# Kernel optimization log

Measured on AMD Instinct MI355X. Metric: run time of the kernel, lower is better.

The kernel has to match this reference:

```python
import jax, jax.numpy as jnp
import numpy as np

B, S, T = 4, 512, 512
V, D, F, H, DK, N = 32000, 512, 2048, 8, 64, 6
PAD = 0

# sinusoidal positional encoding table, matching the torch source exactly
_pos = np.arange(max(S, T))[:, None]
_i = np.arange(D // 2)[None, :]
_ang = _pos / (10000.0 ** (2 * _i / D))
_pe = np.empty((max(S, T), D), dtype=np.float32)
_pe[:, 0::2] = np.sin(_ang)
_pe[:, 1::2] = np.cos(_ang)
PE = jnp.asarray(_pe)


def setup_inputs() -> dict:
    key = jax.random.key(0)
    ks = iter(jax.random.split(key, 64))
    s = 0.02
    w = lambda shape: jax.random.normal(next(ks), shape, jnp.float32) * s
    inp = {
        'src': jax.random.randint(next(ks), (B, S), 0, V, jnp.int32),
        'trg': jax.random.randint(next(ks), (B, T), 0, V, jnp.int32),
        'emb_src': w((V, D)).at[PAD].set(0.0),
        'emb_trg': w((V, D)).at[PAD].set(0.0),
        # encoder stacks (leading axis = layer)
        'enc_wq': w((N, D, H * DK)), 'enc_wk': w((N, D, H * DK)),
        'enc_wv': w((N, D, H * DK)), 'enc_wo': w((N, H * DK, D)),
        'enc_ln1_g': jnp.ones((N, D)), 'enc_ln1_b': jnp.zeros((N, D)),
        'enc_w1': w((N, D, F)), 'enc_b1': jnp.zeros((N, F)),
        'enc_w2': w((N, F, D)), 'enc_b2': jnp.zeros((N, D)),
        'enc_ln2_g': jnp.ones((N, D)), 'enc_ln2_b': jnp.zeros((N, D)),
        # decoder stacks
        'dec_wq': w((N, D, H * DK)), 'dec_wk': w((N, D, H * DK)),
        'dec_wv': w((N, D, H * DK)), 'dec_wo': w((N, H * DK, D)),
        'dec_ln1_g': jnp.ones((N, D)), 'dec_ln1_b': jnp.zeros((N, D)),
        'dec_cq': w((N, D, H * DK)), 'dec_ck': w((N, D, H * DK)),
        'dec_cv': w((N, D, H * DK)), 'dec_co': w((N, H * DK, D)),
        'dec_ln2_g': jnp.ones((N, D)), 'dec_ln2_b': jnp.zeros((N, D)),
        'dec_w1': w((N, D, F)), 'dec_b1': jnp.zeros((N, F)),
        'dec_w2': w((N, F, D)), 'dec_b2': jnp.zeros((N, D)),
        'dec_ln3_g': jnp.ones((N, D)), 'dec_ln3_b': jnp.zeros((N, D)),
        'proj': w((D, V)),
    }
    return inp


def _ln(x, g, b, eps=1e-5):
    m = x.mean(-1, keepdims=True)
    v = ((x - m) ** 2).mean(-1, keepdims=True)
    return (x - m) * jax.lax.rsqrt(v + eps) * g + b


def _mha(xq, xkv, wq, wk, wv, wo, mask):
    b, lq, _ = xq.shape
    lk = xkv.shape[1]
    q = (xq @ wq).reshape(b, lq, H, DK).transpose(0, 2, 1, 3)   # bhqd
    k = (xkv @ wk).reshape(b, lk, H, DK).transpose(0, 2, 1, 3)  # bhkd
    v = (xkv @ wv).reshape(b, lk, H, DK).transpose(0, 2, 1, 3)  # bhkd
    scores = jnp.einsum('bhqd,bhkd->bhqk', q, k)
    scores = jnp.where(mask, -jnp.inf, scores)
    attn = jax.nn.softmax(scores * (DK ** -0.5), axis=-1)
    out = jnp.einsum('bhqk,bhkd->bhqd', attn, v)
    out = out.transpose(0, 2, 1, 3).reshape(b, lq, H * DK)
    return out @ wo


def _ffn(x, w1, b1, w2, b2):
    return jax.nn.relu(x @ w1 + b1) @ w2 + b2


def reference(src, trg, emb_src, emb_trg,
              enc_wq, enc_wk, enc_wv, enc_wo, enc_ln1_g, enc_ln1_b,
              enc_w1, enc_b1, enc_w2, enc_b2, enc_ln2_g, enc_ln2_b,
              dec_wq, dec_wk, dec_wv, dec_wo, dec_ln1_g, dec_ln1_b,
              dec_cq, dec_ck, dec_cv, dec_co, dec_ln2_g, dec_ln2_b,
              dec_w1, dec_b1, dec_w2, dec_b2, dec_ln3_g, dec_ln3_b,
              proj):
    scale = D ** 0.5
    src_pad = (src == PAD)[:, None, None, :]                 # [B,1,1,S]
    trg_pad = (trg == PAD)[:, None, None, :]                 # [B,1,1,T]
    causal = jnp.triu(jnp.ones((T, T), bool), 1)[None, None]  # [1,1,T,T]
    trg_mask = trg_pad | causal

    # encoder (dropout = identity in eval)
    x = emb_src[src] * scale + PE[None, :S]

    def enc_step(h, p):
        wq, wk, wv, wo, g1, b1, w1, bb1, w2, bb2, g2, b2 = p
        h = _ln(h + _mha(h, h, wq, wk, wv, wo, src_pad), g1, b1)
        h = _ln(h + _ffn(h, w1, bb1, w2, bb2), g2, b2)
        return h, None

    x_enc, _ = jax.lax.scan(enc_step, x,
        (enc_wq, enc_wk, enc_wv, enc_wo, enc_ln1_g, enc_ln1_b,
         enc_w1, enc_b1, enc_w2, enc_b2, enc_ln2_g, enc_ln2_b))

    # decoder
    y = emb_trg[trg] * scale + PE[None, :T]

    def dec_step(h, p):
        (wq, wk, wv, wo, g1, b1, cq, ck, cv, co, g2, b2,
         w1, bb1, w2, bb2, g3, b3) = p
        h = _ln(h + _mha(h, h, wq, wk, wv, wo, trg_mask), g1, b1)
        h = _ln(h + _mha(h, x_enc, cq, ck, cv, co, src_pad), g2, b2)
        h = _ln(h + _ffn(h, w1, bb1, w2, bb2), g3, b3)
        return h, None

    y, _ = jax.lax.scan(dec_step, y,
        (dec_wq, dec_wk, dec_wv, dec_wo, dec_ln1_g, dec_ln1_b,
         dec_cq, dec_ck, dec_cv, dec_co, dec_ln2_g, dec_ln2_b,
         dec_w1, dec_b1, dec_w2, dec_b2, dec_ln3_g, dec_ln3_b))

    return y @ proj  # [B, T, trg_vocab]
```

## Files before the change

### kernel.cpp

```cpp
#include <hip/hip_runtime.h>
#include <math.h>

#define BBATCH 4
#define SS 512
#define DDIM 512
#define FFN 2048
#define NHEAD 8
#define DHEAD 64
#define NL 6
#define NVOC 32000
#define MTOK (BBATCH*SS)
#define PAD_ID 0
#define MSZE ((size_t)MTOK * DDIM)

typedef unsigned short u16;
typedef __attribute__((ext_vector_type(8))) short short8;
typedef __attribute__((ext_vector_type(4))) float f32x4;

__device__ __forceinline__ u16 f2bf(float f) {
    union { float f; unsigned u; } v; v.f = f;
    unsigned r = ((v.u >> 16) & 1u) + 0x7fffu;
    return (u16)((v.u + r) >> 16);
}

// ... 67 lines not shown
    auto comp = [&](int t) {
        const u16* as = AsB + (t & 3) * (BM * 32);
        const u16* bs = BsB + (t & 3) * (BN * 32);
        short8 af[MF], bf[NF];
        #pragma unroll
        for (int m = 0; m < MF; m++) {
            int row = wr * (BM / 2) + m * 16 + (lane & 15);
            int slot = ((lane >> 4) << 4) ^ ((row & 3) << 4);
            af[m] = *(const short8*)&as[row * 32 + (slot >> 1)];
        }
        #pragma unroll
        for (int n = 0; n < NF; n++) {
            int row = wc * (BN / 2) + n * 16 + (lane & 15);
            int slot = ((lane >> 4) << 4) ^ ((row & 3) << 4);
            bf[n] = *(const short8*)&bs[row * 32 + (slot >> 1)];
        }
        __builtin_amdgcn_s_setprio(1);
        #pragma unroll
        for (int m = 0; m < MF; m++)
            #pragma unroll
            for (int n = 0; n < NF; n++)
                acc[m][n] = __builtin_amdgcn_mfma_f32_16x16x32_bf16(af[m], bf[n], acc[m][n], 0, 0, 0);
        __builtin_amdgcn_s_setprio(0);
    };

    const int nt = K / 32;
    issue(0); issue(1); issue(2);
    int t = 0;
    for (; t < nt - 2; ++t) {
        waitv<2 * LPT>();
        rawbar();
        if (t + 3 < nt) issue(t + 3);
        comp(t);
    }
    waitv<LPT>(); rawbar(); comp(nt - 2);
    waitv<0>();   rawbar(); comp(nt - 1);

    const int crow = row0 + wr * (BM / 2);
    const int ccol = col0 + wc * (BN / 2);
    #pragma unroll
    for (int m = 0; m < MF; m++) {
        #pragma unroll
        for (int n = 0; n < NF; n++) {
            int col = ccol + n * 16 + (lane & 15);
            float bv = BIAS ? bias[col] : 0.0f;
            #pragma unroll
            for (int i = 0; i < 4; i++) {
                int row = crow + m * 16 + ((lane >> 4) << 2) + i;
                float v = acc[m][n][i] + bv;
                if (RELU) v = fmaxf(v, 0.0f);
                if (OUTBF) ((u16*)Cv)[(size_t)row * ldc + col] = f2bf(v);
                else       ((float*)Cv)[(size_t)row * ldc + col] = v;
            }
        }
    }
}

template<int BM, int BN, int OUTBF, int RELU, int BIAS, int SWZ = 0>
__global__ __launch_bounds__(256) void mgemm(
    const u16* __restrict__ A, int lda, size_t aSb, size_t aSh,
    const u16* __restrict__ B, int ldb, size_t bSb, size_t bSh,
    void* __restrict__ Cv, int ldc, size_t cSb, size_t cSh,
    int K, const float* __restrict__ bias)
{
    __shared__ __align__(16) u16 As[4 * BM * 32];
    __shared__ __align__(16) u16 Bs[4 * BN * 32];
    int bx = blockIdx.x, by = blockIdx.y;
    if (SWZ) {
        int nwg = gridDim.x * gridDim.y;
        int lin = by * gridDim.x + bx;
        int cpx = nwg >> 3;
        int s = (lin & 7) * cpx + (lin >> 3);
        bx = s % gridDim.x; by = s / gridDim.x;
    }
    const int zb = blockIdx.z >> 3, zh = blockIdx.z & 7;
    const u16* Ab = A + (size_t)zb * aSb + (size_t)zh * aSh;
    const u16* Bb = B + (size_t)zb * bSb + (size_t)zh * bSh;
    void* Cb = OUTBF ? (void*)((u16*)Cv + (size_t)zb * cSb + (size_t)zh * cSh)
                     : (void*)((float*)Cv + (size_t)zb * cSb + (size_t)zh * cSh);
    gemm_core<BM, BN, OUTBF, RELU, BIAS>(As, Bs, Ab, lda, Bb, ldb, Cb, ldc,
                                          by * BM, bx * BN, K, bias);
}

template<int BM, int BN>
__global__ __launch_bounds__(256) void mgemm_dual(
    const u16* __restrict__ A1, int lda1, const u16* __restrict__ B1, int ldb1,
    u16* __restrict__ C1, int ldc1, int nx1, int nblk1,
    const u16* __restrict__ A2, int lda2, const u16* __restrict__ B2, int ldb2,
    u16* __restrict__ C2, int ldc2, int nx2,
    int K)
{
    __shared__ __align__(16) u16 As[4 * BM * 32];
    __shared__ __align__(16) u16 Bs[4 * BN * 32];
    int id = blockIdx.x;
    if (id < nblk1) {
        gemm_core<BM, BN, 1, 0, 0>(As, Bs, A1, lda1, B1, ldb1, C1, ldc1,
                                    (id / nx1) * BM, (id % nx1) * BN, K, nullptr);
    } else {
        id -= nblk1;
        gemm_core<BM, BN, 1, 0, 0>(As, Bs, A2, lda2, B2, ldb2, C2, ldc2,
                                    (id / nx2) * BM, (id % nx2) * BN, K, nullptr);
    }
}

__global__ __launch_bounds__(256) void cross_kv(
    const u16* __restrict__ Xb, const u16* __restrict__ Wd,
    u16* __restrict__ Kcr, u16* __restrict__ Vtc)
{
    __shared__ __align__(16) u16 As[4 * 64 * 32];
    __shared__ __align__(16) u16 Bs[4 * 64 * 32];
    int id = blockIdx.x;
    if (id < 1536) {
        int l = id >> 8, t = id & 255;
        const u16* w = Wd + (size_t)l * 4194304u + 1310720u;
        gemm_core<64, 64, 1, 0, 0>(As, Bs, Xb, 512, w, 512,
            Kcr + (size_t)l * MTOK * 512, 512, (t >> 3) * 64, (t & 7) * 64, 512, nullptr);
    } else {
        id -= 1536;
        int l = id >> 8, t = id & 255;
        const u16* w = Wd + (size_t)l * 4194304u + 1572864u;
        gemm_core<64, 64, 1, 0, 0>(As, Bs, w, 512, Xb, 512,
            Vtc + (size_t)l * 512 * MTOK, MTOK, (t >> 5) * 64, (t & 31) * 64, 512, nullptr);
    }
}

template<int CAUSAL>
__global__ __launch_bounds__(256) void flash_attn(
    const u16* __restrict__ Qp, int ldq,
    const u16* __restrict__ Kp, int ldk,
    const u16* __restrict__ Vtp,
    u16* __restrict__ O,
    const int* __restrict__ ids)
{
    __shared__ __align__(16) u16 Kl[3][64 * 64];
    __shared__ __align__(16) u16 Vl[3][64 * 64];
    __shared__ __align__(16) u16 Pl[4][16 * 64];
    __shared__ float msk[SS];

    const int tid = threadIdx.x, lane = tid & 63, wid = tid >> 6;
    const int qt = blockIdx.x, bh = blockIdx.y;
    const int b = bh >> 3, h = bh & 7;
    const int q0 = qt * 64;

    for (int i = tid; i < SS; i += 256)
        msk[i] = (ids[b * SS + i] == PAD_ID) ? -1e30f : 0.0f;

    const int qloc = wid * 16 + (lane & 15);
    const u16* Qb = Qp + (size_t)(b * SS + q0 + qloc) * ldq + h * 64 + ((lane >> 4) * 8);
    short8 qf[2];
    qf[0] = *(const short8*)(Qb);
    qf[1] = *(const short8*)(Qb + 32);

    const u16* Kb = Kp + (size_t)b * SS * ldk + h * 64;
    const u16* Vb = Vtp + (size_t)(h * 64) * MTOK + b * SS;

    auto stage = [&](int buf, int kt) {
        int row = tid >> 3, sl = tid & 7;
        #pragma unroll
        for (int r = 0; r < 2; r++) {
            int rr = row + r * 32;
            int ls = sl ^ (rr & 7);
            gload16(Kb + (size_t)(kt * 64 + rr) * ldk + ls * 8, &Kl[buf][rr * 64 + sl * 8]);
            gload16(Vb + (size_t)rr * MTOK + kt * 64 + ls * 8, &Vl[buf][rr * 64 + sl * 8]);
        }
    };

    const int nt = CAUSAL ? (qt + 1) : (SS / 64);

    float m_i[4], l_i[4];
    f32x4 o_acc[4];
    const f32x4 zero = {0.f, 0.f, 0.f, 0.f};
    #pragma unroll
    for (int i = 0; i < 4; i++) { m_i[i] = -1e30f; l_i[i] = 0.0f; }
    #pragma unroll
    for (int n = 0; n < 4; n++) o_acc[n] = zero;

    auto comp = [&](int kt) {
        const int cur = kt % 3;
        f32x4 s_acc[4];
        #pragma unroll
        for (int n = 0; n < 4; n++) s_acc[n] = zero;
        __builtin_amdgcn_s_setprio(1);
        #pragma unroll
        for (int kk = 0; kk < 2; kk++) {
            #pragma unroll
            for (int n = 0; n < 4; n++) {
                int row = n * 16 + (lane & 15);
                int ls = (kk * 4 + (lane >> 4)) ^ (row & 7);
                short8 kf = *(const short8*)&Kl[cur][row * 64 + ls * 8];
                s_acc[n] = __builtin_amdgcn_mfma_f32_16x16x32_bf16(qf[kk], kf, s_acc[n], 0, 0, 0);
            }
        }
        __builtin_amdgcn_s_setprio(0);

        float sv[4][4];
        #pragma unroll
        for (int n = 0; n < 4; n++) {
            int kg = kt * 64 + n * 16 + (lane & 15);
            float mk = msk[kg];
            #pragma unroll
            for (int i = 0; i < 4; i++) {
                float s = s_acc[n][i] * 0.125f + mk;
                if (CAUSAL) {
                    int qg = q0 + wid * 16 + ((lane >> 4) << 2) + i;
                    if (kg > qg) s = -1e30f;
                }
                sv[n][i] = s;
            }
        }
        float pm[4], mn[4], rs[4], ps[4];
        #pragma unroll
        for (int i = 0; i < 4; i++)
            pm[i] = fmaxf(fmaxf(sv[0][i], sv[1][i]), fmaxf(sv[2][i], sv[3][i]));
        #pragma unroll
        for (int i = 0; i < 4; i++) {
            #pragma unroll
            for (int msh = 1; msh <= 8; msh <<= 1)
                pm[i] = fmaxf(pm[i], __shfl_xor(pm[i], msh));
            mn[i] = fmaxf(m_i[i], pm[i]);
            rs[i] = __expf(m_i[i] - mn[i]);
            m_i[i] = mn[i];
        }
        float p[4][4];
        #pragma unroll
        for (int n = 0; n < 4; n++)
            #pragma unroll
            for (int i = 0; i < 4; i++)
                p[n][i] = (sv[n][i] < -1e29f) ? 0.0f : __expf(sv[n][i] - mn[i]);
        #pragma unroll
        for (int i = 0; i < 4; i++) {
            ps[i] = p[0][i] + p[1][i] + p[2][i] + p[3][i];
            #pragma unroll
            for (int msh = 1; msh <= 8; msh <<= 1)
                ps[i] += __shfl_xor(ps[i], msh);
            l_i[i] = l_i[i] * rs[i] + ps[i];
        }
        #pragma unroll
        for (int n = 0; n < 4; n++)
            #pragma unroll
            for (int i = 0; i < 4; i++)
                o_acc[n][i] *= rs[i];

        #pragma unroll
        for (int n = 0; n < 4; n++) {
            int k = n * 16 + (lane & 15);
            #pragma unroll
            for (int i = 0; i < 4; i++) {
                int q = ((lane >> 4) << 2) + i;
                Pl[wid][q * 64 + (((k >> 3) ^ (q & 7)) << 3) + (k & 7)] = f2bf(p[n][i]);
            }
        }
        asm volatile("s_waitcnt lgkmcnt(0)" ::: "memory");
        __builtin_amdgcn_sched_barrier(0);

        __builtin_amdgcn_s_setprio(1);
        #pragma unroll
        for (int kk = 0; kk < 2; kk++) {
            int qrow = lane & 15;
            int lsp = (kk * 4 + (lane >> 4)) ^ (qrow & 7);
            short8 pa = *(const short8*)&Pl[wid][qrow * 64 + lsp * 8];
            #pragma unroll
            for (int nf = 0; nf < 4; nf++) {
                int row = nf * 16 + (lane & 15);
                int vs = (kk * 4 + (lane >> 4)) ^ (row & 7);
                short8 vf = *(const short8*)&Vl[cur][row * 64 + vs * 8];
                o_acc[nf] = __builtin_amdgcn_mfma_f32_16x16x32_bf16(pa, vf, o_acc[nf], 0, 0, 0);
            }
        }
        __builtin_amdgcn_s_setprio(0);
    };

    stage(0, 0);
    stage(1, 1);
    int t = 0;
    for (; t < nt - 1; ++t) {
        waitv<4>();
        rawbar();
        if (t + 2 < nt) stage((t + 2) % 3, t + 2);
        comp(t);
    }
    waitv<0>(); rawbar(); comp(nt - 1);

    #pragma unroll
    for (int nf = 0; nf < 4; nf++) {
        int d = h * 64 + nf * 16 + (lane & 15);
        #pragma unroll
        for (int i = 0; i < 4; i++) {
            int qg = b * SS + q0 + wid * 16 + ((lane >> 4) << 2) + i;
            O[(size_t)qg * DDIM + d] = f2bf(o_acc[nf][i] / l_i[i]);
        }
    }
}

__device__ __forceinline__ void transp_core(const float* __restrict__ src, u16* __restrict__ dst,
                                            int N, int K, int n0, int k0)
{
    __shared__ u16 t[64][65];
    const int tid = threadIdx.x;
    #pragma unroll
    for (int i = 0; i < 16; i++) {
        int idx = tid + i * 256;
        int kr = idx >> 6, nc = idx & 63;
        t[kr][nc] = f2bf(src[(size_t)(k0 + kr) * N + n0 + nc]);
    }
    __syncthreads();
    #pragma unroll
    for (int i = 0; i < 16; i++) {
        int idx = tid + i * 256;
        int nr = idx >> 6, kc = idx & 63;
        dst[(size_t)(n0 + nr) * K + k0 + kc] = t[kc][nr];
    }
}

__global__ __launch_bounds__(256) void transp(const float* __restrict__ src, u16* __restrict__ dst,
                                              int N, int K, size_t sStride, size_t dStride)
{
    transp_core(src + (size_t)blockIdx.z * sStride, dst + (size_t)blockIdx.z * dStride,
                N, K, blockIdx.x * 64, blockIdx.y * 64);
}

#define OFF_QK 0u
#define OFF_WV 524288u
#define OFF_WO 786432u
#define OFF_CQ 1048576u
#define OFF_CK 1310720u
#define OFF_CV 1572864u
#define OFF_CO 1835008u
#define OFF_W1 2097152u
#define OFF_W2 3145728u
#define WBLK   4194304u
#define M2CNT  262144u
#define MF1CNT 1048576u

__global__ __launch_bounds__(256) void transp_all(
    const float* p0, const float* p1, const float* p2, const float* p3,
    const float* p4, const float* p5, const float* p6, const float* p7,
    const float* p8, const float* p9, const float* p10, const float* p11,
    const float* ew1, const float* dw1, const float* ew2, const float* dw2,
    const float* proj, u16* __restrict__ wreg, u16* __restrict__ projT,
    const int* __restrict__ src, const int* __restrict__ trg,
    const float* __restrict__ es, const float* __restrict__ et,
    float* __restrict__ X, u16* __restrict__ Xb,
    float* __restrict__ Y, u16* __restrict__ Ybf)
{
    int jid = blockIdx.x;
    if (jid < 4608) {
        int z = jid >> 6, t = jid & 63;
        int w = z % 12, l = z / 12;
        const float* ptrs[12] = {p0,p1,p2,p3,p4,p5,p6,p7,p8,p9,p10,p11};
        const float* srcw = ptrs[w] + (size_t)l * M2CNT;
        u16* dst = wreg + (w < 4 ? (size_t)l * WBLK + (size_t)w * M2CNT
                                 : (size_t)(NL + l) * WBLK + (size_t)(w - 4) * M2CNT);
        transp_core(srcw, dst, 512, 512, (t & 7) * 64, (t >> 3) * 64);
    } else if (jid < 7680) {
        int j = jid - 4608;
        int z = j >> 8, t = j & 255;
        int l = z % NL, w = z / NL;
        const float* srcw = (w ? dw1 : ew1) + (size_t)l * MF1CNT;
        u16* dst = wreg + (size_t)(w * NL + l) * WBLK + OFF_W1;
        transp_core(srcw, dst, 2048, 512, (t % 32) * 64, (t / 32) * 64);
    } else if (jid < 10752) {
        int j = jid - 7680;
        int z = j >> 8, t = j & 255;
        int l = z % NL, w = z / NL;
        const float* srcw = (w ? dw2 : ew2) + (size_t)l * MF1CNT;
        u16* dst = wreg + (size_t)(w * NL + l) * WBLK + OFF_W2;
        transp_core(srcw, dst, 512, 2048, (t % 8) * 64, (t / 8) * 64);
    } else if (jid < 14752) {
        int j = jid - 10752;
        transp_core(proj, projT, NVOC, 512, (j % 500) * 64, (j / 500) * 64);
    } else {
        int tok = jid - 14752;
        bool dec = tok >= MTOK;
        int tk = dec ? tok - MTOK : tok;
        int pos = tk & (SS - 1);
        int id2 = (dec ? trg : src)[tk];
        const float* emb = dec ? et : es;
        float* xo = dec ? Y : X;
        u16*   bo = dec ? Ybf : Xb;
        #pragma unroll
        for (int half = 0; half < 2; half++) {
            int d = threadIdx.x + half * 256;
            int i = d >> 1;
            double freq = exp(-(2.0 * (double)i / (double)DDIM) * log(10000.0));
            double ang = (double)pos * freq;
            float pe = (float)((d & 1) ? cos(ang) : sin(ang));
            float val = emb[(size_t)id2 * DDIM + d] * 22.62741699796952f + pe;
            xo[(size_t)tk * DDIM + d] = val;
            bo[(size_t)tk * DDIM + d] = f2bf(val);
        }
    }
}

__global__ void embed_kernel(const int* __restrict__ src, const int* __restrict__ trg,
                             const float* __restrict__ es, const float* __restrict__ et,
                             float* __restrict__ X, u16* __restrict__ Xb,
                             float* __restrict__ Y, u16* __restrict__ Ybf)
{
    int gtok = blockIdx.x;
    int d = threadIdx.x;
    bool dec = gtok >= MTOK;
    int tok = dec ? gtok - MTOK : gtok;
    int pos = tok & (SS - 1);
    int id = (dec ? trg : src)[tok];
    const float* emb = dec ? et : es;
    int i = d >> 1;
    double freq = exp(-(2.0 * (double)i / (double)DDIM) * log(10000.0));
    double ang = (double)pos * freq;
    float pe = (float)((d & 1) ? cos(ang) : sin(ang));
    float val = emb[(size_t)id * DDIM + d] * 22.62741699796952f + pe;
    (dec ? Y : X)[(size_t)tok * DDIM + d] = val;
    (dec ? Ybf : Xb)[(size_t)tok * DDIM + d] = f2bf(val);
}

template<int NP, int BIAS>
__global__ __launch_bounds__(256) void add_ln_rd(float* __restrict__ x,
    const float* __restrict__ part, const float* __restrict__ bias,
    const float* __restrict__ g, const float* __restrict__ bta, u16* __restrict__ xb)
{
    int row = blockIdx.x;
    int tid = threadIdx.x;
    size_t base = (size_t)row * DDIM;
    __shared__ float sbuf[4];

    float v0 = x[base + tid]       + (BIAS ? bias[tid] : 0.0f);
    float v1 = x[base + tid + 256] + (BIAS ? bias[tid + 256] : 0.0f);
    #pragma unroll
    for (int s4 = 0; s4 < NP; s4++) {
        v0 += part[s4 * MSZE + base + tid];
        v1 += part[s4 * MSZE + base + tid + 256];
    }

    float s = v0 + v1;
    #pragma unroll
    for (int o = 32; o > 0; o >>= 1) s += __shfl_down(s, o);
    if ((tid & 63) == 0) sbuf[tid >> 6] = s;
    __syncthreads();
    float mean = (sbuf[0] + sbuf[1] + sbuf[2] + sbuf[3]) * (1.0f / DDIM);
    __syncthreads();

    float d0 = v0 - mean, d1 = v1 - mean;
    float ss = d0 * d0 + d1 * d1;
    #pragma unroll
    for (int o = 32; o > 0; o >>= 1) ss += __shfl_down(ss, o);
    if ((tid & 63) == 0) sbuf[tid >> 6] = ss;
    __syncthreads();
    float var = (sbuf[0] + sbuf[1] + sbuf[2] + sbuf[3]) * (1.0f / DDIM);
    float inv = rsqrtf(var + 1e-5f);

    float o0 = d0 * inv * g[tid]       + bta[tid];
    float o1 = d1 * inv * g[tid + 256] + bta[tid + 256];
    x[base + tid] = o0;
    x[base + tid + 256] = o1;
    xb[base + tid] = f2bf(o0);
    xb[base + tid + 256] = f2bf(o1);
}

extern "C" void kernel_launch(void* const* d_in, const int* in_sizes, int n_in,
                              void* d_out, int out_size, void* d_ws, size_t ws_size,
                              hipStream_t stream)
{
    (void)in_sizes; (void)n_in; (void)out_size;

    const int*   src      = (const int*)  d_in[0];
    const int*   trg      = (const int*)  d_in[1];
    const float* emb_src  = (const float*)d_in[2];
    const float* emb_trg  = (const float*)d_in[3];
    const float* enc_wq   = (const float*)d_in[4];
    const float* enc_wk   = (const float*)d_in[5];
    const float* enc_wv   = (const float*)d_in[6];
    const float* enc_wo   = (const float*)d_in[7];
    const float* enc_ln1g = (const float*)d_in[8];
    const float* enc_ln1b = (const float*)d_in[9];
    const float* enc_w1   = (const float*)d_in[10];
    const float* enc_b1   = (const float*)d_in[11];
    const float* enc_w2   = (const float*)d_in[12];
    const float* enc_b2   = (const float*)d_in[13];
    const float* enc_ln2g = (const float*)d_in[14];
    const float* enc_ln2b = (const float*)d_in[15];
    const float* dec_wq   = (const float*)d_in[16];
    const float* dec_wk   = (const float*)d_in[17];
    const float* dec_wv   = (const float*)d_in[18];
    const float* dec_wo   = (const float*)d_in[19];
    const float* dec_ln1g = (const float*)d_in[20];
    const float* dec_ln1b = (const float*)d_in[21];
    const float* dec_cq   = (const float*)d_in[22];
    const float* dec_ck   = (const float*)d_in[23];
    const float* dec_cv   = (const float*)d_in[24];
    const float* dec_co   = (const float*)d_in[25];
    const float* dec_ln2g = (const float*)d_in[26];
    const float* dec_ln2b = (const float*)d_in[27];
    const float* dec_w1   = (const float*)d_in[28];
    const float* dec_b1   = (const float*)d_in[29];
    const float* dec_w2   = (const float*)d_in[30];
    const float* dec_b2   = (const float*)d_in[31];
    const float* dec_ln3g = (const float*)d_in[32];
    const float* dec_ln3b = (const float*)d_in[33];
    const float* proj     = (const float*)d_in[34];

    float* OUT = (float*)d_out;
    char* base = (char*)d_ws;

    size_t off = 0;
    auto carve = [&](size_t bytes) { char* p = base + off; off += (bytes + 255) & ~(size_t)255; return p; };

    float* X      = (float*)carve(MSZE * 4);
    float* Yb     = (float*)carve(MSZE * 4);
    u16*   Xb     = (u16*)  carve(MSZE * 2);
    u16*   Ybf    = (u16*)  carve(MSZE * 2);
    u16*   QKb    = (u16*)  carve((size_t)MTOK * 1024 * 2);
    u16*   Vt     = (u16*)  carve((size_t)512 * MTOK * 2);
    u16*   CTX    = (u16*)  carve(MSZE * 2);
    u16*   HFF    = (u16*)  carve((size_t)MTOK * FFN * 2);
    u16*   Kcr    = (u16*)  carve((size_t)NL * MTOK * 512 * 2);
    u16*   Vtc    = (u16*)  carve((size_t)NL * 512 * MTOK * 2);
    u16*   projT  = (u16*)  carve((size_t)NVOC * 512 * 2);
    float* Tp4    = (float*)carve((size_t)4 * MSZE * 4);

    const size_t WFULL_B = (size_t)12 * WBLK * 2;
    bool full = (ws_size >= off + WFULL_B);
    u16* Wreg = (u16*)carve(full ? WFULL_B : (size_t)WBLK * 2);

    auto T = [&](const float* s, u16* d, int Kd, int Nd, size_t ss, size_t ds, int L) {
        transp<<<dim3(Nd / 64, Kd / 64, L), 256, 0, stream>>>(s, d, Nd, Kd, ss, ds);
    };

    if (full) {
        transp_all<<<dim3(18848), 256, 0, stream>>>(
            enc_wq, enc_wk, enc_wv, enc_wo,
            dec_wq, dec_wk, dec_wv, dec_wo,
            dec_cq, dec_ck, dec_cv, dec_co,
            enc_w1, dec_w1, enc_w2, dec_w2,
            proj, Wreg, projT,
            src, trg, emb_src, emb_trg, X, Xb, Yb, Ybf);
    } else {
        T(proj, projT, 512, NVOC, 0, 0, 1);
        embed_kernel<<<2 * MTOK, DDIM, 0, stream>>>(src, trg, emb_src, emb_trg, X, Xb, Yb, Ybf);
    }

    auto self_attn = [&](const u16* xsrc, const u16* wb, const int* mask_ids, int causal) {
        mgemm_dual<64, 64><<<dim3(768), 256, 0, stream>>>(
            xsrc, 512, wb + OFF_QK, 512, QKb, 1024, 16, 512,
            wb + OFF_WV, 512, xsrc, 512, Vt, MTOK, 32,
            512);
        if (causal)
            flash_attn<1><<<dim3(8, 32), 256, 0, stream>>>(QKb, 1024, QKb + 512, 1024, Vt, CTX, mask_ids);
        else
            flash_attn<0><<<dim3(8, 32), 256, 0, stream>>>(QKb, 1024, QKb + 512, 1024, Vt, CTX, mask_ids);
        mgemm<64, 64, 0, 0, 0><<<dim3(8, 32, 2), 256, 0, stream>>>(
            CTX, 512, 0, 256, wb + OFF_WO, 512, 0, 256, Tp4, 512, 0, MSZE, 256, nullptr);
    };

    auto o_proj_sk2 = [&](const u16* a, const u16* w) {
        mgemm<64, 64, 0, 0, 0><<<dim3(8, 32, 2), 256, 0, stream>>>(
            a, 512, 0, 256, w, 512, 0, 256, Tp4, 512, 0, MSZE, 256, nullptr);
    };

    auto ffn = [&](const u16* xsrc, const u16* wb, const float* b1) {
        mgemm<64, 64, 1, 1, 1><<<dim3(32, 32, 1), 256, 0, stream>>>(
            xsrc, 512, 0, 0, wb + OFF_W1, 512, 0, 0, HFF, FFN, 0, 0, 512, b1);
        mgemm<64, 64, 0, 0, 0><<<dim3(8, 32, 4), 256, 0, stream>>>(
            HFF, 2048, 0, 512, wb + OFF_W2, 2048, 0, 512,
            Tp4, 512, 0, MSZE, 512, nullptr);
    };

    const size_t M2 = M2CNT, MF1 = MF1CNT;

    for (int l = 0; l < NL; l++) {
        u16* wb;
        if (full) wb = Wreg + (size_t)l * WBLK;
        else {
            wb = Wreg;
            T(enc_wq + l * M2,  wb + OFF_QK,      512, 512,  0, 0, 1);
            T(enc_wk + l * M2,  wb + OFF_QK + M2, 512, 512,  0, 0, 1);
            T(enc_wv + l * M2,  wb + OFF_WV,      512, 512,  0, 0, 1);
            T(enc_wo + l * M2,  wb + OFF_WO,      512, 512,  0, 0, 1);
            T(enc_w1 + l * MF1, wb + OFF_W1,      512, 2048, 0, 0, 1);
            T(enc_w2 + l * MF1, wb + OFF_W2,      2048, 512, 0, 0, 1);
        }
        self_attn(Xb, wb, src, 0);
        add_ln_rd<2, 0><<<MTOK, 256, 0, stream>>>(X, Tp4, nullptr,
            enc_ln1g + l * DDIM, enc_ln1b + l * DDIM, Xb);
        ffn(Xb, wb, enc_b1 + l * FFN);
        add_ln_rd<4, 1><<<MTOK, 256, 0, stream>>>(X, Tp4, enc_b2 + l * DDIM,
            enc_ln2g + l * DDIM, enc_ln2b + l * DDIM, Xb);
    }

    if (full) {
        cross_kv<<<dim3(3072), 256, 0, stream>>>(Xb, Wreg + (size_t)NL * WBLK, Kcr, Vtc);
    }

    for (int l = 0; l < NL; l++) {
        u16* wb;
        if (full) wb = Wreg + (size_t)(NL + l) * WBLK;
        else {
            wb = Wreg;
            T(dec_wq + l * M2,  wb + OFF_QK,      512, 512,  0, 0, 1);
            T(dec_wk + l * M2,  wb + OFF_QK + M2, 512, 512,  0, 0, 1);
            T(dec_wv + l * M2,  wb + OFF_WV,      512, 512,  0, 0, 1);
            T(dec_wo + l * M2,  wb + OFF_WO,      512, 512,  0, 0, 1);
            T(dec_cq + l * M2,  wb + OFF_CQ,      512, 512,  0, 0, 1);
            T(dec_ck + l * M2,  wb + OFF_CK,      512, 512,  0, 0, 1);
            T(dec_cv + l * M2,  wb + OFF_CV,      512, 512,  0, 0, 1);
            T(dec_co + l * M2,  wb + OFF_CO,      512, 512,  0, 0, 1);
            T(dec_w1 + l * MF1, wb + OFF_W1,      512, 2048, 0, 0, 1);
            T(dec_w2 + l * MF1, wb + OFF_W2,      2048, 512, 0, 0, 1);
            mgemm<64, 64, 1, 0, 0><<<dim3(8, 32, 1), 256, 0, stream>>>(
                Xb, 512, 0, 0, wb + OFF_CK, 512, 0, 0, Kcr + (size_t)l * MTOK * 512, 512, 0, 0, 512, nullptr);
            mgemm<64, 64, 1, 0, 0><<<dim3(32, 8, 1), 256, 0, stream>>>(
                wb + OFF_CV, 512, 0, 0, Xb, 512, 0, 0, Vtc + (size_t)l * 512 * MTOK, MTOK, 0, 0, 512, nullptr);
        }
        self_attn(Ybf, wb, trg, 1);
        add_ln_rd<2, 0><<<MTOK, 256, 0, stream>>>(Yb, Tp4, nullptr,
            dec_ln1g + l * DDIM, dec_ln1b + l * DDIM, Ybf);
        mgemm<64, 64, 1, 0, 0><<<dim3(8, 32, 1), 256, 0, stream>>>(
            Ybf, 512, 0, 0, wb + OFF_CQ, 512, 0, 0, QKb, 1024, 0, 0, 512, nullptr);
        flash_attn<0><<<dim3(8, 32), 256, 0, stream>>>(
            QKb, 1024, Kcr + (size_t)l * MTOK * 512, 512, Vtc + (size_t)l * 512 * MTOK, CTX, src);
        o_proj_sk2(CTX, wb + OFF_CO);
        add_ln_rd<2, 0><<<MTOK, 256, 0, stream>>>(Yb, Tp4, nullptr,
            dec_ln2g + l * DDIM, dec_ln2b + l * DDIM, Ybf);
        ffn(Ybf, wb, dec_b1 + l * FFN);
        add_ln_rd<4, 1><<<MTOK, 256, 0, stream>>>(Yb, Tp4, dec_b2 + l * DDIM,
            dec_ln3g + l * DDIM, dec_ln3b + l * DDIM, Ybf);
    }

    mgemm<128, 128, 0, 0, 0, 1><<<dim3(NVOC / 128, MTOK / 128, 1), 256, 0, stream>>>(
        Ybf, 512, 0, 0, projT, 512, 0, 0, OUT, NVOC, 0, 0, 512, nullptr);
}
```

Baseline: 1.432 ms.

## Co-schedule encoder layer 0 with decoder layer 0 self-attention in merged kernels

Decoder layer 0's self-attention block depends only on the target embedding, not on the encoder output. This change runs it concurrently with encoder layer 0 by merging their QKV projections, flash attention, output projections and layernorms into paired launches. The decoder cross-attention Q projection is folded into the encoder FFN1 launch. The aim is fewer launches and better GPU fill on small grids, at the cost of extra scratch buffers and more complex control flow.

```diff
diff --git a/kernel.cpp b/kernel.cpp
--- a/kernel.cpp
+++ b/kernel.cpp
@@ -173,241 +173,25 @@
                                           by * BM, bx * BN, K, bias);
 }
 
-template<int BM, int BN>
+template<int BM, int BN, int RELU1 = 0, int BIAS1 = 0>
 __global__ __launch_bounds__(256) void mgemm_dual(
     const u16* __restrict__ A1, int lda1, const u16* __restrict__ B1, int ldb1,
     u16* __restrict__ C1, int ldc1, int nx1, int nblk1,
     const u16* __restrict__ A2, int lda2, const u16* __restrict__ B2, int ldb2,
     u16* __restrict__ C2, int ldc2, int nx2,
-    int K)
+    int K, const float* __restrict__ bias1)
 {
     __shared__ __align__(16) u16 As[4 * BM * 32];
     __shared__ __align__(16) u16 Bs[4 * BN * 32];
     int id = blockIdx.x;
     if (id < nblk1) {
-        gemm_core<BM, BN, 1, 0, 0>(As, Bs, A1, lda1, B1, ldb1, C1, ldc1,
-                                    (id / nx1) * BM, (id % nx1) * BN, K, nullptr);
+        gemm_core<BM, BN, 1, RELU1, BIAS1>(As, Bs, A1, lda1, B1, ldb1, C1, ldc1,
+                                            (id / nx1) * BM, (id % nx1) * BN, K, bias1);
     } else {
         id -= nblk1;
         gemm_core<BM, BN, 1, 0, 0>(As, Bs, A2, lda2, B2, ldb2, C2, ldc2,
                                     (id / nx2) * BM, (id % nx2) * BN, K, nullptr);
     }
-}
-
-__global__ __launch_bounds__(256) void cross_kv(
-    const u16* __restrict__ Xb, const u16* __restrict__ Wd,
-    u16* __restrict__ Kcr, u16* __restrict__ Vtc)
-{
-    __shared__ __align__(16) u16 As[4 * 64 * 32];
-    __shared__ __align__(16) u16 Bs[4 * 64 * 32];
-    int id = blockIdx.x;
-    if (id < 1536) {
-        int l = id >> 8, t = id & 255;
-        const u16* w = Wd + (size_t)l * 4194304u + 1310720u;
-        gemm_core<64, 64, 1, 0, 0>(As, Bs, Xb, 512, w, 512,
-            Kcr + (size_t)l * MTOK * 512, 512, (t >> 3) * 64, (t & 7) * 64, 512, nullptr);
-    } else {
-        id -= 1536;
-        int l = id >> 8, t = id & 255;
-        const u16* w = Wd + (size_t)l * 4194304u + 1572864u;
-        gemm_core<64, 64, 1, 0, 0>(As, Bs, w, 512, Xb, 512,
-            Vtc + (size_t)l * 512 * MTOK, MTOK, (t >> 5) * 64, (t & 31) * 64, 512, nullptr);
-    }
-}
-
-template<int CAUSAL>
-__global__ __launch_bounds__(256) void flash_attn(
-    const u16* __restrict__ Qp, int ldq,
-    const u16* __restrict__ Kp, int ldk,
-    const u16* __restrict__ Vtp,
-    u16* __restrict__ O,
-    const int* __restrict__ ids)
-{
-    __shared__ __align__(16) u16 Kl[3][64 * 64];
-    __shared__ __align__(16) u16 Vl[3][64 * 64];
-    __shared__ __align__(16) u16 Pl[4][16 * 64];
-    __shared__ float msk[SS];
-
-    const int tid = threadIdx.x, lane = tid & 63, wid = tid >> 6;
-    const int qt = blockIdx.x, bh = blockIdx.y;
-    const int b = bh >> 3, h = bh & 7;
-    const int q0 = qt * 64;
-
-    for (int i = tid; i < SS; i += 256)
-        msk[i] = (ids[b * SS + i] == PAD_ID) ? -1e30f : 0.0f;
-
-    const int qloc = wid * 16 + (lane & 15);
-    const u16* Qb = Qp + (size_t)(b * SS + q0 + qloc) * ldq + h * 64 + ((lane >> 4) * 8);
-    short8 qf[2];
-    qf[0] = *(const short8*)(Qb);
-    qf[1] = *(const short8*)(Qb + 32);
-
-    const u16* Kb = Kp + (size_t)b * SS * ldk + h * 64;
-    const u16* Vb = Vtp + (size_t)(h * 64) * MTOK + b * SS;
-
-    auto stage = [&](int buf, int kt) {
-        int row = tid >> 3, sl = tid & 7;
-        #pragma unroll
-        for (int r = 0; r < 2; r++) {
-            int rr = row + r * 32;
-            int ls = sl ^ (rr & 7);
-            gload16(Kb + (size_t)(kt * 64 + rr) * ldk + ls * 8, &Kl[buf][rr * 64 + sl * 8]);
-            gload16(Vb + (size_t)rr * MTOK + kt * 64 + ls * 8, &Vl[buf][rr * 64 + sl * 8]);
-        }
-    };
-
-    const int nt = CAUSAL ? (qt + 1) : (SS / 64);
-
-    float m_i[4], l_i[4];
-    f32x4 o_acc[4];
-    const f32x4 zero = {0.f, 0.f, 0.f, 0.f};
-    #pragma unroll
-    for (int i = 0; i < 4; i++) { m_i[i] = -1e30f; l_i[i] = 0.0f; }
-    #pragma unroll
-    for (int n = 0; n < 4; n++) o_acc[n] = zero;
-
-    auto comp = [&](int kt) {
-        const int cur = kt % 3;
-        f32x4 s_acc[4];
-        #pragma unroll
-        for (int n = 0; n < 4; n++) s_acc[n] = zero;
-        __builtin_amdgcn_s_setprio(1);
-        #pragma unroll
-        for (int kk = 0; kk < 2; kk++) {
-            #pragma unroll
-            for (int n = 0; n < 4; n++) {
-                int row = n * 16 + (lane & 15);
-                int ls = (kk * 4 + (lane >> 4)) ^ (row & 7);
-                short8 kf = *(const short8*)&Kl[cur][row * 64 + ls * 8];
-                s_acc[n] = __builtin_amdgcn_mfma_f32_16x16x32_bf16(qf[kk], kf, s_acc[n], 0, 0, 0);
-            }
-        }
-        __builtin_amdgcn_s_setprio(0);
-
-        float sv[4][4];
-        #pragma unroll
-        for (int n = 0; n < 4; n++) {
-            int kg = kt * 64 + n * 16 + (lane & 15);
-            float mk = msk[kg];
-            #pragma unroll
-            for (int i = 0; i < 4; i++) {
-                float s = s_acc[n][i] * 0.125f + mk;
-                if (CAUSAL) {
-                    int qg = q0 + wid * 16 + ((lane >> 4) << 2) + i;
-                    if (kg > qg) s = -1e30f;
-                }
-                sv[n][i] = s;
-            }
-        }
-        float pm[4], mn[4], rs[4], ps[4];
-        #pragma unroll
-        for (int i = 0; i < 4; i++)
-            pm[i] = fmaxf(fmaxf(sv[0][i], sv[1][i]), fmaxf(sv[2][i], sv[3][i]));
-        #pragma unroll
-        for (int i = 0; i < 4; i++) {
-            #pragma unroll
-            for (int msh = 1; msh <= 8; msh <<= 1)
-                pm[i] = fmaxf(pm[i], __shfl_xor(pm[i], msh));
-            mn[i] = fmaxf(m_i[i], pm[i]);
-            rs[i] = __expf(m_i[i] - mn[i]);
-            m_i[i] = mn[i];
-        }
-        float p[4][4];
-        #pragma unroll
-        for (int n = 0; n < 4; n++)
-            #pragma unroll
-            for (int i = 0; i < 4; i++)
-                p[n][i] = (sv[n][i] < -1e29f) ? 0.0f : __expf(sv[n][i] - mn[i]);
-        #pragma unroll
-        for (int i = 0; i < 4; i++) {
-            ps[i] = p[0][i] + p[1][i] + p[2][i] + p[3][i];
-            #pragma unroll
-            for (int msh = 1; msh <= 8; msh <<= 1)
-                ps[i] += __shfl_xor(ps[i], msh);
-            l_i[i] = l_i[i] * rs[i] + ps[i];
-        }
-        #pragma unroll
-        for (int n = 0; n < 4; n++)
-            #pragma unroll
-            for (int i = 0; i < 4; i++)
-                o_acc[n][i] *= rs[i];
-
-        #pragma unroll
-        for (int n = 0; n < 4; n++) {
-            int k = n * 16 + (lane & 15);
-            #pragma unroll
-            for (int i = 0; i < 4; i++) {
-                int q = ((lane >> 4) << 2) + i;
-                Pl[wid][q * 64 + (((k >> 3) ^ (q & 7)) << 3) + (k & 7)] = f2bf(p[n][i]);
-            }
-        }
-        asm volatile("s_waitcnt lgkmcnt(0)" ::: "memory");
-        __builtin_amdgcn_sched_barrier(0);
-
-        __builtin_amdgcn_s_setprio(1);
-        #pragma unroll
-        for (int kk = 0; kk < 2; kk++) {
-            int qrow = lane & 15;
-            int lsp = (kk * 4 + (lane >> 4)) ^ (qrow & 7);
-            short8 pa = *(const short8*)&Pl[wid][qrow * 64 + lsp * 8];
-            #pragma unroll
-            for (int nf = 0; nf < 4; nf++) {
-                int row = nf * 16 + (lane & 15);
-                int vs = (kk * 4 + (lane >> 4)) ^ (row & 7);
-                short8 vf = *(const short8*)&Vl[cur][row * 64 + vs * 8];
-                o_acc[nf] = __builtin_amdgcn_mfma_f32_16x16x32_bf16(pa, vf, o_acc[nf], 0, 0, 0);
-            }
-        }
-        __builtin_amdgcn_s_setprio(0);
-    };
-
-    stage(0, 0);
-    stage(1, 1);
-    int t = 0;
-    for (; t < nt - 1; ++t) {
-        waitv<4>();
-        rawbar();
-        if (t + 2 < nt) stage((t + 2) % 3, t + 2);
-        comp(t);
-    }
-    waitv<0>(); rawbar(); comp(nt - 1);
-
-    #pragma unroll
-    for (int nf = 0; nf < 4; nf++) {
-        int d = h * 64 + nf * 16 + (lane & 15);
-        #pragma unroll
-        for (int i = 0; i < 4; i++) {
-            int qg = b * SS + q0 + wid * 16 + ((lane >> 4) << 2) + i;
-            O[(size_t)qg * DDIM + d] = f2bf(o_acc[nf][i] / l_i[i]);
-        }
-    }
-}
-
-__device__ __forceinline__ void transp_core(const float* __restrict__ src, u16* __restrict__ dst,
-                                            int N, int K, int n0, int k0)
-{
-    __shared__ u16 t[64][65];
-    const int tid = threadIdx.x;
-    #pragma unroll
-    for (int i = 0; i < 16; i++) {
-        int idx = tid + i * 256;
-        int kr = idx >> 6, nc = idx & 63;
-        t[kr][nc] = f2bf(src[(size_t)(k0 + kr) * N + n0 + nc]);
-    }
-    __syncthreads();
-    #pragma unroll
-    for (int i = 0; i < 16; i++) {
-        int idx = tid + i * 256;
-        int nr = idx >> 6, kc = idx & 63;
-        dst[(size_t)(n0 + nr) * K + k0 + kc] = t[kc][nr];
-    }
-}
-
-__global__ __launch_bounds__(256) void transp(const float* __restrict__ src, u16* __restrict__ dst,
-                                              int N, int K, size_t sStride, size_t dStride)
-{
-    transp_core(src + (size_t)blockIdx.z * sStride, dst + (size_t)blockIdx.z * dStride,
-                N, K, blockIdx.x * 64, blockIdx.y * 64);
 }
 
 #define OFF_QK 0u
@@ -422,6 +206,289 @@
 #define WBLK   4194304u
 #define M2CNT  262144u
 #define MF1CNT 1048576u
+
+__global__ __launch_bounds__(256) void qkv_quad(
+    const u16* __restrict__ Xb, const u16* __restrict__ Ybf,
+    const u16* __restrict__ We, const u16* __restrict__ Wd0,
+    u16* __restrict__ QKb, u16* __restrict__ Vt,
+    u16* __restrict__ QKb2, u16* __restrict__ Vt2)
+{
+    __shared__ __align__(16) u16 As[4 * 64 * 32];
+    __shared__ __align__(16) u16 Bs[4 * 64 * 32];
+    int id = blockIdx.x;
+    if (id < 512)
+        gemm_core<64,64,1,0,0>(As, Bs, Xb, 512, We + OFF_QK, 512, QKb, 1024,
+                               (id >> 4) * 64, (id & 15) * 64, 512, nullptr);
+    else if (id < 768) {
+        int t = id - 512;
+        gemm_core<64,64,1,0,0>(As, Bs, We + OFF_WV, 512, Xb, 512, Vt, MTOK,
+                               (t >> 5) * 64, (t & 31) * 64, 512, nullptr);
+    } else if (id < 1280) {
+        int t = id - 768;
+        gemm_core<64,64,1,0,0>(As, Bs, Ybf, 512, Wd0 + OFF_QK, 512, QKb2, 1024,
+                               (t >> 4) * 64, (t & 15) * 64, 512, nullptr);
+    } else {
+        int t = id - 1280;
+        gemm_core<64,64,1,0,0>(As, Bs, Wd0 + OFF_WV, 512, Ybf, 512, Vt2, MTOK,
+                               (t >> 5) * 64, (t & 31) * 64, 512, nullptr);
+    }
+}
+
+__global__ __launch_bounds__(256) void oproj_pair(
+    const u16* __restrict__ CTX, const u16* __restrict__ We,
+    const u16* __restrict__ CTX2, const u16* __restrict__ Wd0,
+    float* __restrict__ Tp4)
+{
+    __shared__ __align__(16) u16 As[4 * 64 * 32];
+    __shared__ __align__(16) u16 Bs[4 * 64 * 32];
+    int id = blockIdx.x;
+    int which = id >> 9;
+    int kh = (id >> 8) & 1;
+    int t = id & 255;
+    const u16* A = (which ? CTX2 : CTX) + kh * 256;
+    const u16* W = (which ? Wd0 + OFF_WO : We + OFF_WO) + kh * 256;
+    float* out = Tp4 + (size_t)(which * 2 + kh) * MSZE;
+    gemm_core<64,64,0,0,0>(As, Bs, A, 512, W, 512, out, 512,
+                           (t >> 3) * 64, (t & 7) * 64, 256, nullptr);
+}
+
+__global__ __launch_bounds__(256) void cross_kv(
+    const u16* __restrict__ Xb, const u16* __restrict__ Wd,
+    u16* __restrict__ Kcr, u16* __restrict__ Vtc)
+{
+    __shared__ __align__(16) u16 As[4 * 64 * 32];
+    __shared__ __align__(16) u16 Bs[4 * 64 * 32];
+    int id = blockIdx.x;
+    if (id < 1536) {
+        int l = id >> 8, t = id & 255;
+        const u16* w = Wd + (size_t)l * WBLK + OFF_CK;
+        gemm_core<64, 64, 1, 0, 0>(As, Bs, Xb, 512, w, 512,
+            Kcr + (size_t)l * MTOK * 512, 512, (t >> 3) * 64, (t & 7) * 64, 512, nullptr);
+    } else {
+        id -= 1536;
+        int l = id >> 8, t = id & 255;
+        const u16* w = Wd + (size_t)l * WBLK + OFF_CV;
+        gemm_core<64, 64, 1, 0, 0>(As, Bs, w, 512, Xb, 512,
+            Vtc + (size_t)l * 512 * MTOK, MTOK, (t >> 5) * 64, (t & 31) * 64, 512, nullptr);
+    }
+}
+
+__device__ __forceinline__ void flash_body(char* smem, int causal, int qt, int bh,
+    const u16* __restrict__ Qp, int ldq,
+    const u16* __restrict__ Kp, int ldk,
+    const u16* __restrict__ Vtp,
+    u16* __restrict__ O, const int* __restrict__ ids)
+{
+    u16* Kl = (u16*)smem;
+    u16* Vl = Kl + 12288;
+    u16* Pl = Vl + 12288;
+    float* msk = (float*)(Pl + 4096);
+
+    const int tid = threadIdx.x, lane = tid & 63, wid = tid >> 6;
+    const int b = bh >> 3, h = bh & 7;
+    const int q0 = qt * 64;
+
+    for (int i = tid; i < SS; i += 256)
+        msk[i] = (ids[b * SS + i] == PAD_ID) ? -1e30f : 0.0f;
+
+    const int qloc = wid * 16 + (lane & 15);
+    const u16* Qb = Qp + (size_t)(b * SS + q0 + qloc) * ldq + h * 64 + ((lane >> 4) * 8);
+    short8 qf[2];
+    qf[0] = *(const short8*)(Qb);
+    qf[1] = *(const short8*)(Qb + 32);
+
+    const u16* Kb = Kp + (size_t)b * SS * ldk + h * 64;
+    const u16* Vb = Vtp + (size_t)(h * 64) * MTOK + b * SS;
+
+    auto stage = [&](int buf, int kt) {
+        int row = tid >> 3, sl = tid & 7;
+        #pragma unroll
+        for (int r = 0; r < 2; r++) {
+            int rr = row + r * 32;
+            int ls = sl ^ (rr & 7);
+            gload16(Kb + (size_t)(kt * 64 + rr) * ldk + ls * 8, &Kl[buf * 4096 + rr * 64 + sl * 8]);
+            gload16(Vb + (size_t)rr * MTOK + kt * 64 + ls * 8, &Vl[buf * 4096 + rr * 64 + sl * 8]);
+        }
+    };
+
+    const int nt = causal ? (qt + 1) : (SS / 64);
+
+    float m_i[4], l_i[4];
+    f32x4 o_acc[4];
+    const f32x4 zero = {0.f, 0.f, 0.f, 0.f};
+    #pragma unroll
+    for (int i = 0; i < 4; i++) { m_i[i] = -1e30f; l_i[i] = 0.0f; }
+    #pragma unroll
+    for (int n = 0; n < 4; n++) o_acc[n] = zero;
+
+    auto comp = [&](int kt) {
+        const int cur = kt % 3;
+        f32x4 s_acc[4];
+        #pragma unroll
+        for (int n = 0; n < 4; n++) s_acc[n] = zero;
+        __builtin_amdgcn_s_setprio(1);
+        #pragma unroll
+        for (int kk = 0; kk < 2; kk++) {
+            #pragma unroll
+            for (int n = 0; n < 4; n++) {
+                int row = n * 16 + (lane & 15);
+                int ls = (kk * 4 + (lane >> 4)) ^ (row & 7);
+                short8 kf = *(const short8*)&Kl[cur * 4096 + row * 64 + ls * 8];
+                s_acc[n] = __builtin_amdgcn_mfma_f32_16x16x32_bf16(qf[kk], kf, s_acc[n], 0, 0, 0);
+            }
+        }
+        __builtin_amdgcn_s_setprio(0);
+
+        float sv[4][4];
+        #pragma unroll
+        for (int n = 0; n < 4; n++) {
+            int kg = kt * 64 + n * 16 + (lane & 15);
+            float mk = msk[kg];
+            #pragma unroll
+            for (int i = 0; i < 4; i++) {
+                float s = s_acc[n][i] * 0.125f + mk;
+                if (causal) {
+                    int qg = q0 + wid * 16 + ((lane >> 4) << 2) + i;
+                    if (kg > qg) s = -1e30f;
+                }
+                sv[n][i] = s;
+            }
+        }
+        float pm[4], mn[4], rs[4], ps[4];
+        #pragma unroll
+        for (int i = 0; i < 4; i++)
+            pm[i] = fmaxf(fmaxf(sv[0][i], sv[1][i]), fmaxf(sv[2][i], sv[3][i]));
+        #pragma unroll
+        for (int i = 0; i < 4; i++) {
+            #pragma unroll
+            for (int msh = 1; msh <= 8; msh <<= 1)
+                pm[i] = fmaxf(pm[i], __shfl_xor(pm[i], msh));
+            mn[i] = fmaxf(m_i[i], pm[i]);
+            rs[i] = __expf(m_i[i] - mn[i]);
+            m_i[i] = mn[i];
+        }
+        float p[4][4];
+        #pragma unroll
+        for (int n = 0; n < 4; n++)
+            #pragma unroll
+            for (int i = 0; i < 4; i++)
+                p[n][i] = (sv[n][i] < -1e29f) ? 0.0f : __expf(sv[n][i] - mn[i]);
+        #pragma unroll
+        for (int i = 0; i < 4; i++) {
+            ps[i] = p[0][i] + p[1][i] + p[2][i] + p[3][i];
+            #pragma unroll
+            for (int msh = 1; msh <= 8; msh <<= 1)
+                ps[i] += __shfl_xor(ps[i], msh);
+            l_i[i] = l_i[i] * rs[i] + ps[i];
+        }
+        #pragma unroll
+        for (int n = 0; n < 4; n++)
+            #pragma unroll
+            for (int i = 0; i < 4; i++)
+                o_acc[n][i] *= rs[i];
+
+        #pragma unroll
+        for (int n = 0; n < 4; n++) {
+            int k = n * 16 + (lane & 15);
+            #pragma unroll
+            for (int i = 0; i < 4; i++) {
+                int q = ((lane >> 4) << 2) + i;
+                Pl[wid * 1024 + q * 64 + (((k >> 3) ^ (q & 7)) << 3) + (k & 7)] = f2bf(p[n][i]);
+            }
+        }
+        asm volatile("s_waitcnt lgkmcnt(0)" ::: "memory");
+        __builtin_amdgcn_sched_barrier(0);
+
+        __builtin_amdgcn_s_setprio(1);
+        #pragma unroll
+        for (int kk = 0; kk < 2; kk++) {
+            int qrow = lane & 15;
+            int lsp = (kk * 4 + (lane >> 4)) ^ (qrow & 7);
+            short8 pa = *(const short8*)&Pl[wid * 1024 + qrow * 64 + lsp * 8];
+            #pragma unroll
+            for (int nf = 0; nf < 4; nf++) {
+                int row = nf * 16 + (lane & 15);
+                int vs = (kk * 4 + (lane >> 4)) ^ (row & 7);
+                short8 vf = *(const short8*)&Vl[cur * 4096 + row * 64 + vs * 8];
+                o_acc[nf] = __builtin_amdgcn_mfma_f32_16x16x32_bf16(pa, vf, o_acc[nf], 0, 0, 0);
+            }
+        }
+        __builtin_amdgcn_s_setprio(0);
+    };
+
+    stage(0, 0);
+    stage(1, 1);
+    int t = 0;
+    for (; t < nt - 1; ++t) {
+        waitv<4>();
+        rawbar();
+        if (t + 2 < nt) stage((t + 2) % 3, t + 2);
+        comp(t);
+    }
+    waitv<0>(); rawbar(); comp(nt - 1);
+
+    #pragma unroll
+    for (int nf = 0; nf < 4; nf++) {
+        int d = h * 64 + nf * 16 + (lane & 15);
+        #pragma unroll
+        for (int i = 0; i < 4; i++) {
+            int qg = b * SS + q0 + wid * 16 + ((lane >> 4) << 2) + i;
+            O[(size_t)qg * DDIM + d] = f2bf(o_acc[nf][i] / l_i[i]);
+        }
+    }
+}
+
+template<int CAUSAL>
+__global__ __launch_bounds__(256) void flash_attn(
+    const u16* __restrict__ Qp, int ldq,
+    const u16* __restrict__ Kp, int ldk,
+    const u16* __restrict__ Vtp,
+    u16* __restrict__ O,
+    const int* __restrict__ ids)
+{
+    __shared__ __align__(16) char smem[59392];
+    flash_body(smem, CAUSAL, blockIdx.x, blockIdx.y, Qp, ldq, Kp, ldk, Vtp, O, ids);
+}
+
+__global__ __launch_bounds__(256) void flash_pair(
+    const u16* __restrict__ QKb, const u16* __restrict__ Vt, u16* __restrict__ CTX,
+    const int* __restrict__ src,
+    const u16* __restrict__ QKb2, const u16* __restrict__ Vt2, u16* __restrict__ CTX2,
+    const int* __restrict__ trg)
+{
+    __shared__ __align__(16) char smem[59392];
+    if (blockIdx.y < 32)
+        flash_body(smem, 0, blockIdx.x, blockIdx.y, QKb, 1024, QKb + 512, 1024, Vt, CTX, src);
+    else
+        flash_body(smem, 1, blockIdx.x, blockIdx.y - 32, QKb2, 1024, QKb2 + 512, 1024, Vt2, CTX2, trg);
+}
+
+__device__ __forceinline__ void transp_core(const float* __restrict__ src, u16* __restrict__ dst,
+                                            int N, int K, int n0, int k0)
+{
+    __shared__ u16 t[64][65];
+    const int tid = threadIdx.x;
+    #pragma unroll
+    for (int i = 0; i < 16; i++) {
+        int idx = tid + i * 256;
+        int kr = idx >> 6, nc = idx & 63;
+        t[kr][nc] = f2bf(src[(size_t)(k0 + kr) * N + n0 + nc]);
+    }
+    __syncthreads();
+    #pragma unroll
+    for (int i = 0; i < 16; i++) {
+        int idx = tid + i * 256;
+        int nr = idx >> 6, kc = idx & 63;
+        dst[(size_t)(n0 + nr) * K + k0 + kc] = t[kc][nr];
+    }
+}
+
+__global__ __launch_bounds__(256) void transp(const float* __restrict__ src, u16* __restrict__ dst,
+                                              int N, int K, size_t sStride, size_t dStride)
+{
+    transp_core(src + (size_t)blockIdx.z * sStride, dst + (size_t)blockIdx.z * dStride,
+                N, K, blockIdx.x * 64, blockIdx.y * 64);
+}
 
 __global__ __launch_bounds__(256) void transp_all(
     const float* p0, const float* p1, const float* p2, const float* p3,
@@ -504,23 +571,15 @@
     (dec ? Ybf : Xb)[(size_t)tok * DDIM + d] = f2bf(val);
 }
 
-template<int NP, int BIAS>
-__global__ __launch_bounds__(256) void add_ln_rd(float* __restrict__ x,
-    const float* __restrict__ part, const float* __restrict__ bias,
-    const float* __restrict__ g, const float* __restrict__ bta, u16* __restrict__ xb)
-{
-    int row = blockIdx.x;
+__device__ __forceinline__ void ln2_body(float* __restrict__ x, const float* __restrict__ part,
+    const float* __restrict__ g, const float* __restrict__ bta, u16* __restrict__ xb, int row)
+{
     int tid = threadIdx.x;
     size_t base = (size_t)row * DDIM;
     __shared__ float sbuf[4];
 
-    float v0 = x[base + tid]       + (BIAS ? bias[tid] : 0.0f);
-    float v1 = x[base + tid + 256] + (BIAS ? bias[tid + 256] : 0.0f);
-    #pragma unroll
-    for (int s4 = 0; s4 < NP; s4++) {
-        v0 += part[s4 * MSZE + base + tid];
-        v1 += part[s4 * MSZE + base + tid + 256];
-    }
+    float v0 = x[base + tid]       + part[base + tid]       + part[MSZE + base + tid];
+    float v1 = x[base + tid + 256] + part[base + tid + 256] + part[MSZE + base + tid + 256];
 
     float s = v0 + v1;
     #pragma unroll
@@ -545,6 +604,61 @@
     x[base + tid + 256] = o1;
     xb[base + tid] = f2bf(o0);
     xb[base + tid + 256] = f2bf(o1);
+}
+
+template<int NP, int BIAS>
+__global__ __launch_bounds__(256) void add_ln_rd(float* __restrict__ x,
+    const float* __restrict__ part, const float* __restrict__ bias,
+    const float* __restrict__ g, const float* __restrict__ bta, u16* __restrict__ xb)
+{
+    int row = blockIdx.x;
+    int tid = threadIdx.x;
+    size_t base = (size_t)row * DDIM;
+    __shared__ float sbuf[4];
+
+    float v0 = x[base + tid]       + (BIAS ? bias[tid] : 0.0f);
+    float v1 = x[base + tid + 256] + (BIAS ? bias[tid + 256] : 0.0f);
+    #pragma unroll
+    for (int s4 = 0; s4 < NP; s4++) {
+        v0 += part[s4 * MSZE + base + tid];
+        v1 += part[s4 * MSZE + base + tid + 256];
+    }
+
+    float s = v0 + v1;
+    #pragma unroll
+    for (int o = 32; o > 0; o >>= 1) s += __shfl_down(s, o);
+    if ((tid & 63) == 0) sbuf[tid >> 6] = s;
+    __syncthreads();
+    float mean = (sbuf[0] + sbuf[1] + sbuf[2] + sbuf[3]) * (1.0f / DDIM);
+    __syncthreads();
+
+    float d0 = v0 - mean, d1 = v1 - mean;
+    float ss = d0 * d0 + d1 * d1;
+    #pragma unroll
+    for (int o = 32; o > 0; o >>= 1) ss += __shfl_down(ss, o);
+    if ((tid & 63) == 0) sbuf[tid >> 6] = ss;
+    __syncthreads();
+    float var = (sbuf[0] + sbuf[1] + sbuf[2] + sbuf[3]) * (1.0f / DDIM);
+    float inv = rsqrtf(var + 1e-5f);
+
+    float o0 = d0 * inv * g[tid]       + bta[tid];
+    float o1 = d1 * inv * g[tid + 256] + bta[tid + 256];
+    x[base + tid] = o0;
+    x[base + tid + 256] = o1;
+    xb[base + tid] = f2bf(o0);
+    xb[base + tid + 256] = f2bf(o1);
+}
+
+__global__ __launch_bounds__(256) void add_ln_pair(
+    float* __restrict__ X, u16* __restrict__ Xb,
+    const float* __restrict__ eg, const float* __restrict__ eb,
+    float* __restrict__ Y, u16* __restrict__ Ybf,
+    const float* __restrict__ dg, const float* __restrict__ db,
+    const float* __restrict__ Tp4)
+{
+    int row = blockIdx.x;
+    if (row < MTOK) ln2_body(X, Tp4, eg, eb, Xb, row);
+    else            ln2_body(Y, Tp4 + 2 * MSZE, dg, db, Ybf, row - MTOK);
 }
 
 extern "C" void kernel_launch(void* const* d_in, const int* in_sizes, int n_in,
@@ -600,8 +714,11 @@
     u16*   Xb     = (u16*)  carve(MSZE * 2);
     u16*   Ybf    = (u16*)  carve(MSZE * 2);
     u16*   QKb    = (u16*)  carve((size_t)MTOK * 1024 * 2);
+    u16*   QKb2   = (u16*)  carve((size_t)MTOK * 1024 * 2);
     u16*   Vt     = (u16*)  carve((size_t)512 * MTOK * 2);
+    u16*   Vt2    = (u16*)  carve((size_t)512 * MTOK * 2);
     u16*   CTX    = (u16*)  carve(MSZE * 2);
+    u16*   CTX2   = (u16*)  carve(MSZE * 2);
     u16*   HFF    = (u16*)  carve((size_t)MTOK * FFN * 2);
     u16*   Kcr    = (u16*)  carve((size_t)NL * MTOK * 512 * 2);
     u16*   Vtc    = (u16*)  carve((size_t)NL * 512 * MTOK * 2);
@@ -633,7 +750,7 @@
         mgemm_dual<64, 64><<<dim3(768), 256, 0, stream>>>(
             xsrc, 512, wb + OFF_QK, 512, QKb, 1024, 16, 512,
             wb + OFF_WV, 512, xsrc, 512, Vt, MTOK, 32,
-            512);
+            512, nullptr);
         if (causal)
             flash_attn<1><<<dim3(8, 32), 256, 0, stream>>>(QKb, 1024, QKb + 512, 1024, Vt, CTX, mask_ids);
         else
@@ -656,8 +773,27 @@
     };
 
     const size_t M2 = M2CNT, MF1 = MF1CNT;
-
-    for (int l = 0; l < NL; l++) {
+    u16* Wd0 = Wreg + (size_t)NL * WBLK;
+
+    if (full) {
+        u16* we = Wreg;
+        qkv_quad<<<dim3(1536), 256, 0, stream>>>(Xb, Ybf, we, Wd0, QKb, Vt, QKb2, Vt2);
+        flash_pair<<<dim3(8, 64), 256, 0, stream>>>(QKb, Vt, CTX, src, QKb2, Vt2, CTX2, trg);
+        oproj_pair<<<dim3(1024), 256, 0, stream>>>(CTX, we, CTX2, Wd0, Tp4);
+        add_ln_pair<<<dim3(2 * MTOK), 256, 0, stream>>>(
+            X, Xb, enc_ln1g, enc_ln1b, Yb, Ybf, dec_ln1g, dec_ln1b, Tp4);
+        mgemm_dual<64, 64, 1, 1><<<dim3(1280), 256, 0, stream>>>(
+            Xb, 512, we + OFF_W1, 512, HFF, FFN, 32, 1024,
+            Ybf, 512, Wd0 + OFF_CQ, 512, QKb2, 1024, 8,
+            512, enc_b1);
+        mgemm<64, 64, 0, 0, 0><<<dim3(8, 32, 4), 256, 0, stream>>>(
+            HFF, 2048, 0, 512, we + OFF_W2, 2048, 0, 512,
+            Tp4, 512, 0, MSZE, 512, nullptr);
+        add_ln_rd<4, 1><<<MTOK, 256, 0, stream>>>(X, Tp4, enc_b2,
+            enc_ln2g, enc_ln2b, Xb);
+    }
+
+    for (int l = full ? 1 : 0; l < NL; l++) {
         u16* wb;
         if (full) wb = Wreg + (size_t)l * WBLK;
         else {
@@ -678,7 +814,7 @@
     }
 
     if (full) {
-        cross_kv<<<dim3(3072), 256, 0, stream>>>(Xb, Wreg + (size_t)NL * WBLK, Kcr, Vtc);
+        cross_kv<<<dim3(3072), 256, 0, stream>>>(Xb, Wd0, Kcr, Vtc);
     }
 
     for (int l = 0; l < NL; l++) {
@@ -701,13 +837,17 @@
             mgemm<64, 64, 1, 0, 0><<<dim3(32, 8, 1), 256, 0, stream>>>(
                 wb + OFF_CV, 512, 0, 0, Xb, 512, 0, 0, Vtc + (size_t)l * 512 * MTOK, MTOK, 0, 0, 512, nullptr);
         }
-        self_attn(Ybf, wb, trg, 1);
-        add_ln_rd<2, 0><<<MTOK, 256, 0, stream>>>(Yb, Tp4, nullptr,
-            dec_ln1g + l * DDIM, dec_ln1b + l * DDIM, Ybf);
-        mgemm<64, 64, 1, 0, 0><<<dim3(8, 32, 1), 256, 0, stream>>>(
-            Ybf, 512, 0, 0, wb + OFF_CQ, 512, 0, 0, QKb, 1024, 0, 0, 512, nullptr);
+        const bool merged0 = full && (l == 0);
+        if (!merged0) {
+            self_attn(Ybf, wb, trg, 1);
+            add_ln_rd<2, 0><<<MTOK, 256, 0, stream>>>(Yb, Tp4, nullptr,
+                dec_ln1g + l * DDIM, dec_ln1b + l * DDIM, Ybf);
+            mgemm<64, 64, 1, 0, 0><<<dim3(8, 32, 1), 256, 0, stream>>>(
+                Ybf, 512, 0, 0, wb + OFF_CQ, 512, 0, 0, QKb, 1024, 0, 0, 512, nullptr);
+        }
+        const u16* Qsrc = merged0 ? QKb2 : QKb;
         flash_attn<0><<<dim3(8, 32), 256, 0, stream>>>(
-            QKb, 1024, Kcr + (size_t)l * MTOK * 512, 512, Vtc + (size_t)l * 512 * MTOK, CTX, src);
+            Qsrc, 1024, Kcr + (size_t)l * MTOK * 512, 512, Vtc + (size_t)l * 512 * MTOK, CTX, src);
         o_proj_sk2(CTX, wb + OFF_CO);
         add_ln_rd<2, 0><<<MTOK, 256, 0, stream>>>(Yb, Tp4, nullptr,
             dec_ln2g + l * DDIM, dec_ln2b + l * DDIM, Ybf);
```

Result: faster. 1.396 ms (-2.5%).
